# Kernel tuning notes

Hardware: AMD Instinct MI355X
Metric: run time of the kernel (lower is better)

Reference implementation:

```python
import jax, jax.numpy as jnp
import numpy as np
import math

B, S, E = 4, 2048, 1024


def setup_inputs() -> dict:
    key = jax.random.key(0)
    ks = jax.random.split(key, 9)
    x = jax.random.normal(ks[0], (B, S, E), dtype=jnp.float32)
    # causal boolean mask, broadcast over batch: True = keep
    mask = jnp.broadcast_to(jnp.tril(jnp.ones((S, S), dtype=bool)), (B, S, S))
    sc = 1.0 / math.sqrt(E)
    Wq = jax.random.normal(ks[1], (E, E), dtype=jnp.float32) * sc
    bq = jnp.zeros((E,), dtype=jnp.float32)
    Wk = jax.random.normal(ks[2], (E, E), dtype=jnp.float32) * sc
    bk = jnp.zeros((E,), dtype=jnp.float32)
    Wv = jax.random.normal(ks[3], (E, E), dtype=jnp.float32) * sc
    bv = jnp.zeros((E,), dtype=jnp.float32)
    gamma = jnp.ones((E,), dtype=jnp.float32)
    beta = jnp.zeros((E,), dtype=jnp.float32)
    return {"x": x, "mask": mask, "Wq": Wq, "bq": bq, "Wk": Wk, "bk": bk,
            "Wv": Wv, "bv": bv, "gamma": gamma, "beta": beta}


def reference(x, mask, Wq, bq, Wk, bk, Wv, bv, gamma, beta):
    E_ = x.shape[-1]
    q = jnp.einsum('bse,fe->bsf', x, Wq) + bq
    k = jnp.einsum('bse,fe->bsf', x, Wk) + bk
    v = jnp.einsum('bse,fe->bsf', x, Wv) + bv
    scores = jnp.einsum('bqe,bke->bqk', q, k) / jnp.sqrt(jnp.float32(E_))
    scores = jnp.where(mask, scores, -jnp.inf)
    probs = jax.nn.softmax(scores, axis=-1)
    attn = jnp.einsum('bqk,bke->bqe', probs, v)
    y = attn + x
    # LayerNorm over last dim, eps matches torch default 1e-5
    mu = jnp.mean(y, axis=-1, keepdims=True)
    var = jnp.mean(jnp.square(y - mu), axis=-1, keepdims=True)
    return (y - mu) / jnp.sqrt(var + 1e-5) * gamma + beta
```

## Files before the change

kernel.cpp:

```cpp
#include <hip/hip_runtime.h>
#include <hip/hip_bf16.h>
#include <stdint.h>

#define B_ 4
#define S_ 2048
#define E_ 1024
#define BS_ (B_*S_)

using bf16x8 = __attribute__((ext_vector_type(8))) __bf16;
using f32x4  = __attribute__((ext_vector_type(4))) float;

__constant__ int pv_mt[24] = {7,8,9,10,11,12,13,14,15,15,14,6,13,5,12,4,11,3,10,2,9,1,8,0};
__constant__ int pv_ck[24] = {0,0,0,0,0,0,0,0,0, 1, 1,0, 1,0, 1,0, 1,0, 1,0, 1,0, 1,0};

__device__ __forceinline__ unsigned short f2bf(float f) {
  unsigned int u = __float_as_uint(f);
  u += 0x7fffu + ((u >> 16) & 1u);
  return (unsigned short)(u >> 16);
}
__device__ __forceinline__ float bf2f(unsigned short h) {
  return __uint_as_float(((unsigned int)h) << 16);
}

__device__ __forceinline__ void gld16(const unsigned short* g, unsigned short* l) {
  __builtin_amdgcn_global_load_lds((__attribute__((address_space(1))) void*)(void*)g,
                                   (__attribute__((address_space(3))) void*)l, 16, 0, 0);
}

__global__ __launch_bounds__(256) void prep_all(
    const float* __restrict__ x,
    const float* __restrict__ Wq, const float* __restrict__ Wk, const float* __restrict__ Wv,
    const float* __restrict__ bq, const float* __restrict__ bk, const float* __restrict__ bv,
    unsigned short* __restrict__ xb, unsigned short* __restrict__ Wb, float* __restrict__ bb) {
  const int i = blockIdx.x * 256 + threadIdx.x;
  const int nx4 = BS_ * E_ / 4, nw4 = E_ * E_ / 4;
  if (i < nx4) {
    const float4 v = ((const float4*)x)[i];
    ushort4 o;
    o.x = f2bf(v.x); o.y = f2bf(v.y); o.z = f2bf(v.z); o.w = f2bf(v.w);
    ((ushort4*)xb)[i] = o;
  } else if (i < nx4 + 3 * nw4) {
    const int j = i - nx4;
    const int m = j / nw4, jj = j - m * nw4;
    const float* src = (m == 0) ? Wq : (m == 1) ? Wk : Wv;
    const float4 v = ((const float4*)src)[jj];
    ushort4 o;
    o.x = f2bf(v.x); o.y = f2bf(v.y); o.z = f2bf(v.z); o.w = f2bf(v.w);
    ((ushort4*)Wb)[j] = o;
  } else {
    const int j = i - nx4 - 3 * nw4;
    if (j < 3 * E_) bb[j] = (j < E_) ? bq[j] : (j < 2 * E_) ? bk[j - E_] : bv[j - 2 * E_];
  }
}

template<int EPI>
__global__ __launch_bounds__(256, 3) void gemm_bt(
    const unsigned short* __restrict__ A, const unsigned short* __restrict__ Bm,
    float* __restrict__ Cf, float* __restrict__ Cf2,
    unsigned short* __restrict__ Cb, unsigned short* __restrict__ VtOut,
    const float* __restrict__ bias,
    int K, int lda, int ldb, int ldc,
    long sA, long sB, long sC, float scale)
{
  constexpr int BM = 128, BN = 128, BK = 64;
  __shared__ __align__(16) unsigned short As[BM * BK];
  __shared__ __align__(16) unsigned short Bs[BN * BK];

  int mt, nt, ck = 0, bz;
  if (EPI == 1) {
    const int sig = (blockIdx.x & 7) * 68 + (blockIdx.x >> 3);
    bz = sig / 136;
    const int rem = sig - bz * 136;
    const int M = (rem >= 78) ? 3 : (rem >= 36) ? 2 : (rem >= 10) ? 1 : 0;
    const int cumM = (M == 3) ? 78 : (M == 2) ? 36 : (M == 1) ? 10 : 0;
    const int inner = rem - cumM;
    if (inner < 16 * M) {
      const int N = inner >> 4, t2 = inner & 15;
      mt = 4 * M + (t2 >> 2); nt = 4 * N + (t2 & 3);
    } else {
      const int t2 = inner - 16 * M;
      const int ml = (t2 >= 6) ? 3 : (t2 >= 3) ? 2 : (t2 >= 1) ? 1 : 0;
      const int nl = t2 - (ml * (ml + 1)) / 2;
      mt = 4 * M + ml; nt = 4 * M + nl;
    }
  } else if (EPI == 2) {
    mt = pv_mt[blockIdx.y]; ck = pv_ck[blockIdx.y]; nt = blockIdx.x; bz = blockIdx.z;
  } else {
    mt = blockIdx.y; nt = blockIdx.x; bz = blockIdx.z;
  }
  A  += sA * bz;
  Bm += sB * bz;
  const int m0 = mt * BM, n0 = nt * BN;
  const int k0s  = (EPI == 2 && ck) ? 1024 : 0;
  const int kend = (EPI == 2) ? (ck ? m0 + BM : min(1024, m0 + BM)) : K;

  const int t = threadIdx.x;
  const int lane = t & 63, wave = t >> 6;
  const int wr = wave >> 1, wc = wave & 1;
  const int q = lane >> 4, r = lane & 15;

  const int srow   = lane >> 3;
  const int schunk = (lane & 7) ^ srow;
  const long ga0 = (long)(m0 + wave * 32 + srow) * lda + schunk * 8;
  const long gb0 = (long)(n0 + wave * 32 + srow) * ldb + schunk * 8;

  f32x4 acc[4][4] = {};

  for (int k0 = k0s; k0 < kend; k0 += BK) {
#pragma unroll
    for (int s = 0; s < 4; ++s) {
      gld16(A  + ga0 + (long)s * 8 * lda + k0, &As[(wave * 32 + s * 8) * 64]);
      gld16(Bm + gb0 + (long)s * 8 * ldb + k0, &Bs[(wave * 32 + s * 8) * 64]);
    }
    __syncthreads();
#pragma unroll
    for (int kk = 0; kk < BK; kk += 32) {
      bf16x8 af[4], bfr[4];
      const int cq = (kk >> 3) + q;
#pragma unroll
      for (int i = 0; i < 4; ++i) {
        const int row = wr * 64 + i * 16 + r;
        af[i] = *(const bf16x8*)&As[(row * 8 + (cq ^ (r & 7))) * 8];
      }
#pragma unroll
      for (int j = 0; j < 4; ++j) {
        const int row = wc * 64 + j * 16 + r;
        bfr[j] = *(const bf16x8*)&Bs[(row * 8 + (cq ^ (r & 7))) * 8];
      }
#pragma unroll
      for (int i = 0; i < 4; ++i)
#pragma unroll
        for (int j = 0; j < 4; ++j)
          acc[i][j] = __builtin_amdgcn_mfma_f32_16x16x32_bf16(af[i], bfr[j], acc[i][j], 0, 0, 0);
    }
    __syncthreads();
  }

  if (EPI == 0) {
    if (n0 < 2 * E_) {
#pragma unroll
      for (int i = 0; i < 4; ++i)
#pragma unroll
        for (int j = 0; j < 4; ++j) {
          const int col = n0 + wc * 64 + j * 16 + r;
          const float bia = bias[col];
#pragma unroll
          for (int e = 0; e < 4; ++e) {
            const int rowg = m0 + wr * 64 + i * 16 + q * 4 + e;
            Cb[(long)rowg * ldc + col] = f2bf(acc[i][j][e] + bia);
          }
        }
    } else {
      unsigned short* scr = As + wave * 2048;
      const int bb = m0 >> 11;
      const int sbase = (m0 & (S_ - 1)) + wr * 64;
      const float bia = bias[n0 + wc * 64 +  0 + r];
      (void)bia;
#pragma unroll
      for (int j = 0; j < 4; ++j) {
        const int e_base = n0 - 2 * E_ + wc * 64 + j * 16;
        const float bj = bias[n0 + wc * 64 + j * 16 + r];
#pragma unroll
        for (int i = 0; i < 4; ++i) {
          const int c = 2 * i + (q >> 1);
          const int slot = c ^ (r & 7);
          ushort4 o;
          o.x = f2bf(acc[i][j][0] + bj);
          o.y = f2bf(acc[i][j][1] + bj);
          o.z = f2bf(acc[i][j][2] + bj);
          o.w = f2bf(acc[i][j][3] + bj);
          *(ushort4*)&scr[r * 72 + slot * 8 + (q & 1) * 4] = o;
        }
#pragma unroll
        for (int it = 0; it < 2; ++it) {
          const int er = it * 8 + (lane >> 3);
          const int w = lane & 7;
          const bf16x8 vv = *(const bf16x8*)&scr[er * 72 + w * 8];
          const int so = (w ^ (er & 7)) * 8;
          *(bf16x8*)&VtOut[((long)bb * E_ + e_base + er) * S_ + sbase + so] = vv;
        }
      }
    }
  } else if (EPI == 1) {
    Cb += sC * bz;
#pragma unroll
    for (int i = 0; i < 4; ++i)
#pragma unroll
      for (int j = 0; j < 4; ++j) {
        const int col = n0 + wc * 64 + j * 16 + r;
#pragma unroll
        for (int e = 0; e < 4; ++e) {
          const int rowg = m0 + wr * 64 + i * 16 + q * 4 + e;
          Cb[(long)rowg * ldc + col] = f2bf(acc[i][j][e] * scale);
        }
      }
  } else {
    float* dst = (ck ? Cf2 : Cf) + sC * bz;
#pragma unroll
    for (int i = 0; i < 4; ++i)
#pragma unroll
      for (int j = 0; j < 4; ++j) {
        const int col = n0 + wc * 64 + j * 16 + r;
#pragma unroll
        for (int e = 0; e < 4; ++e) {
          const int rowg = m0 + wr * 64 + i * 16 + q * 4 + e;
          dst[(long)rowg * ldc + col] = acc[i][j][e];
        }
      }
  }
}

__global__ __launch_bounds__(256) void softmax_causal(unsigned short* __restrict__ Sc) {
  const int row = blockIdx.x * 4 + (threadIdx.x >> 6);
  const int lane = threadIdx.x & 63;
  const int b = row >> 11, ii = row & (S_ - 1);
  unsigned short* prow = Sc + (long)b * S_ * S_ + (long)ii * S_;
  const int len = ii + 1;
  const int wend = ((ii >> 7) + 1) << 7;
  float v[32];
#pragma unroll
  for (int c = 0; c < 4; ++c) {
    const int base = (c * 64 + lane) * 8;
    if (base < len) {
      const uint4 u = *(const uint4*)&prow[base];
      const unsigned int w[4] = {u.x, u.y, u.z, u.w};
#pragma unroll
      for (int e = 0; e < 8; ++e) {
        const unsigned short h = (unsigned short)(w[e >> 1] >> ((e & 1) * 16));
        v[c * 8 + e] = (base + e < len) ? bf2f(h) : -3.0e38f;
      }
    } else {
#pragma unroll
      for (int e = 0; e < 8; ++e) v[c * 8 + e] = -3.0e38f;
    }
  }
  float mx = -3.0e38f;
#pragma unroll
  for (int i = 0; i < 32; ++i) mx = fmaxf(mx, v[i]);
#pragma unroll
  for (int o = 32; o; o >>= 1) mx = fmaxf(mx, __shfl_xor(mx, o));
  float sum = 0.f;
#pragma unroll
  for (int i = 0; i < 32; ++i) { v[i] = __expf(v[i] - mx); sum += v[i]; }
#pragma unroll
  for (int o = 32; o; o >>= 1) sum += __shfl_xor(sum, o);
  const float inv = 1.0f / sum;
#pragma unroll
  for (int c = 0; c < 4; ++c) {
    const int base = (c * 64 + lane) * 8;
    if (base >= wend) continue;
    uint4 u;
    unsigned int w[4];
#pragma unroll
    for (int p = 0; p < 4; ++p) {
      const unsigned short lo = f2bf(v[c * 8 + p * 2] * inv);
      const unsigned short hi = f2bf(v[c * 8 + p * 2 + 1] * inv);
      w[p] = (unsigned int)lo | ((unsigned int)hi << 16);
    }
    u.x = w[0]; u.y = w[1]; u.z = w[2]; u.w = w[3];
    *(uint4*)&prow[base] = u;
  }
}

__global__ __launch_bounds__(256) void residual_ln(
    const float* __restrict__ attn, const float* __restrict__ attn2,
    const float* __restrict__ x,
    const float* __restrict__ gamma, const float* __restrict__ beta,
    float* __restrict__ out) {
  __shared__ float rs[4], rs2[4];
  const long row = blockIdx.x;
  const int t = threadIdx.x;
  const int lane = t & 63, wave = t >> 6;
  const float4 a  = ((const float4*)(attn + row * E_))[t];
  const float4 xv = ((const float4*)(x + row * E_))[t];
  float4 a2 = make_float4(0.f, 0.f, 0.f, 0.f);
  if ((row & (S_ - 1)) >= 1024) a2 = ((const float4*)(attn2 + row * E_))[t];
  const float y0 = a.x + a2.x + xv.x, y1 = a.y + a2.y + xv.y;
  const float y2 = a.z + a2.z + xv.z, y3 = a.w + a2.w + xv.w;
  float s  = y0 + y1 + y2 + y3;
  float s2 = y0 * y0 + y1 * y1 + y2 * y2 + y3 * y3;
#pragma unroll
  for (int o = 32; o; o >>= 1) { s += __shfl_xor(s, o); s2 += __shfl_xor(s2, o); }
  if (lane == 0) { rs[wave] = s; rs2[wave] = s2; }
  __syncthreads();
  s  = rs[0] + rs[1] + rs[2] + rs[3];
  s2 = rs2[0] + rs2[1] + rs2[2] + rs2[3];
  const float mu  = s * (1.0f / E_);
  const float var = s2 * (1.0f / E_) - mu * mu;
  const float inv = rsqrtf(var + 1e-5f);
  const float4 g  = ((const float4*)gamma)[t];
  const float4 be = ((const float4*)beta)[t];
  float4 o;
  o.x = (y0 - mu) * inv * g.x + be.x;
  o.y = (y1 - mu) * inv * g.y + be.y;
  o.z = (y2 - mu) * inv * g.z + be.z;
  o.w = (y3 - mu) * inv * g.w + be.w;
  ((float4*)(out + row * E_))[t] = o;
}

extern "C" void kernel_launch(void* const* d_in, const int* in_sizes, int n_in,
                              void* d_out, int out_size, void* d_ws, size_t ws_size,
                              hipStream_t stream) {
  const float* x  = (const float*)d_in[0];
  const float* Wq = (const float*)d_in[2];
  const float* bq = (const float*)d_in[3];
  const float* Wk = (const float*)d_in[4];
  const float* bk = (const float*)d_in[5];
  const float* Wv = (const float*)d_in[6];
  const float* bv = (const float*)d_in[7];
  const float* gamma = (const float*)d_in[8];
  const float* beta  = (const float*)d_in[9];
  float* out = (float*)d_out;

  char* ws = (char*)d_ws;
  size_t off = 0;
  auto alloc = [&](size_t bytes) { char* p = ws + off; off += (bytes + 255) & ~(size_t)255; return p; };
  unsigned short* xb    = (unsigned short*)alloc((size_t)BS_ * E_ * 2);
  unsigned short* Wqkvb = (unsigned short*)alloc((size_t)3 * E_ * E_ * 2);
  float*          bqkv  = (float*)alloc((size_t)3 * E_ * 4);
  unsigned short* Cqkv  = (unsigned short*)alloc((size_t)BS_ * 2 * E_ * 2);
  unsigned short* Vt    = (unsigned short*)alloc((size_t)BS_ * E_ * 2);
  unsigned short* Sc    = (unsigned short*)alloc((size_t)B_ * S_ * S_ * 2);
  float*          attn2 = (float*)alloc((size_t)BS_ * E_ * 4);
  float* attn = (float*)Cqkv;

  const int nprep = BS_ * E_ / 4 + 3 * E_ * E_ / 4 + 3 * E_;
  prep_all<<<dim3((nprep + 255) / 256), 256, 0, stream>>>(x, Wq, Wk, Wv, bq, bk, bv, xb, Wqkvb, bqkv);

  dim3 g1(3 * E_ / 128, BS_ / 128, 1);
  gemm_bt<0><<<g1, 256, 0, stream>>>(xb, Wqkvb, nullptr, nullptr, Cqkv, Vt, bqkv,
                                     E_, E_, E_, 2 * E_, 0, 0, 0, 1.f);

  gemm_bt<1><<<dim3(544), 256, 0, stream>>>(Cqkv, Cqkv + E_, nullptr, nullptr, Sc, nullptr, nullptr,
                                            E_, 2 * E_, 2 * E_, S_,
                                            (long)S_ * 2 * E_, (long)S_ * 2 * E_, (long)S_ * S_,
                                            0.03125f);

  softmax_causal<<<dim3(BS_ / 4), 256, 0, stream>>>(Sc);

  dim3 g3(E_ / 128, 24, B_);
  gemm_bt<2><<<g3, 256, 0, stream>>>(Sc, Vt, attn, attn2, nullptr, nullptr, nullptr,
                                     S_, S_, S_, E_,
                                     (long)S_ * S_, (long)S_ * E_, (long)S_ * E_, 1.f);

  residual_ln<<<dim3(BS_), 256, 0, stream>>>(attn, attn2, x, gamma, beta, out);
}
```

Baseline: 277.1 us.

## Fuse causal softmax into QK and PV GEMM epilogues, drop softmax kernel

The score GEMM epilogue now applies the causal mask and writes unnormalized exp(score), without subtracting a row max; the exponent is clamped at 60. Per-row sums are accumulated with atomics into a row-sum buffer that the prep kernel zeroes. The PV GEMM divides by that sum in its epilogue and writes bf16 partial outputs, which the LayerNorm kernel then reads. This removes the separate softmax pass over the score matrix and halves the bytes of the attention intermediates. In exchange it adds atomics and loses numerical safety for large logits, since it relies on scores staying small.

```diff
diff --git a/kernel.cpp b/kernel.cpp
--- a/kernel.cpp
+++ b/kernel.cpp
@@ -31,7 +31,8 @@
     const float* __restrict__ x,
     const float* __restrict__ Wq, const float* __restrict__ Wk, const float* __restrict__ Wv,
     const float* __restrict__ bq, const float* __restrict__ bk, const float* __restrict__ bv,
-    unsigned short* __restrict__ xb, unsigned short* __restrict__ Wb, float* __restrict__ bb) {
+    unsigned short* __restrict__ xb, unsigned short* __restrict__ Wb, float* __restrict__ bb,
+    float* __restrict__ lz) {
   const int i = blockIdx.x * 256 + threadIdx.x;
   const int nx4 = BS_ * E_ / 4, nw4 = E_ * E_ / 4;
   if (i < nx4) {
@@ -50,13 +51,14 @@
   } else {
     const int j = i - nx4 - 3 * nw4;
     if (j < 3 * E_) bb[j] = (j < E_) ? bq[j] : (j < 2 * E_) ? bk[j - E_] : bv[j - 2 * E_];
+    else { const int k = j - 3 * E_; if (k < BS_) lz[k] = 0.f; }
   }
 }
 
 template<int EPI>
 __global__ __launch_bounds__(256, 3) void gemm_bt(
     const unsigned short* __restrict__ A, const unsigned short* __restrict__ Bm,
-    float* __restrict__ Cf, float* __restrict__ Cf2,
+    float* __restrict__ Cf,
     unsigned short* __restrict__ Cb, unsigned short* __restrict__ VtOut,
     const float* __restrict__ bias,
     int K, int lda, int ldb, int ldc,
@@ -154,8 +156,6 @@
       unsigned short* scr = As + wave * 2048;
       const int bb = m0 >> 11;
       const int sbase = (m0 & (S_ - 1)) + wr * 64;
-      const float bia = bias[n0 + wc * 64 +  0 + r];
-      (void)bia;
 #pragma unroll
       for (int j = 0; j < 4; ++j) {
         const int e_base = n0 - 2 * E_ + wc * 64 + j * 16;
@@ -183,87 +183,52 @@
     }
   } else if (EPI == 1) {
     Cb += sC * bz;
-#pragma unroll
-    for (int i = 0; i < 4; ++i)
+    float* lv = Cf + (long)bz * S_;
+#pragma unroll
+    for (int i = 0; i < 4; ++i) {
+      float rs[4] = {0.f, 0.f, 0.f, 0.f};
 #pragma unroll
       for (int j = 0; j < 4; ++j) {
         const int col = n0 + wc * 64 + j * 16 + r;
 #pragma unroll
         for (int e = 0; e < 4; ++e) {
           const int rowg = m0 + wr * 64 + i * 16 + q * 4 + e;
-          Cb[(long)rowg * ldc + col] = f2bf(acc[i][j][e] * scale);
+          float p = 0.f;
+          if (col <= rowg) p = __expf(fminf(acc[i][j][e] * scale, 60.f));
+          Cb[(long)rowg * ldc + col] = f2bf(p);
+          rs[e] += p;
         }
       }
+#pragma unroll
+      for (int e = 0; e < 4; ++e) {
+        float s = rs[e];
+        s += __shfl_xor(s, 1); s += __shfl_xor(s, 2);
+        s += __shfl_xor(s, 4); s += __shfl_xor(s, 8);
+        if (r == 0) atomicAdd(&lv[m0 + wr * 64 + i * 16 + q * 4 + e], s);
+      }
+    }
   } else {
-    float* dst = (ck ? Cf2 : Cf) + sC * bz;
-#pragma unroll
-    for (int i = 0; i < 4; ++i)
+    const float* lv = Cf + (long)bz * S_;
+    unsigned short* dst = (ck ? VtOut : Cb) + sC * bz;
+#pragma unroll
+    for (int i = 0; i < 4; ++i) {
+      const int rb = m0 + wr * 64 + i * 16 + q * 4;
+      const float4 l4 = *(const float4*)&lv[rb];
+      const float r0 = 1.f / l4.x, r1 = 1.f / l4.y, r2 = 1.f / l4.z, r3 = 1.f / l4.w;
 #pragma unroll
       for (int j = 0; j < 4; ++j) {
         const int col = n0 + wc * 64 + j * 16 + r;
-#pragma unroll
-        for (int e = 0; e < 4; ++e) {
-          const int rowg = m0 + wr * 64 + i * 16 + q * 4 + e;
-          dst[(long)rowg * ldc + col] = acc[i][j][e];
-        }
-      }
+        dst[(long)(rb + 0) * ldc + col] = f2bf(acc[i][j][0] * r0);
+        dst[(long)(rb + 1) * ldc + col] = f2bf(acc[i][j][1] * r1);
+        dst[(long)(rb + 2) * ldc + col] = f2bf(acc[i][j][2] * r2);
+        dst[(long)(rb + 3) * ldc + col] = f2bf(acc[i][j][3] * r3);
+      }
+    }
   }
 }
 
-__global__ __launch_bounds__(256) void softmax_causal(unsigned short* __restrict__ Sc) {
-  const int row = blockIdx.x * 4 + (threadIdx.x >> 6);
-  const int lane = threadIdx.x & 63;
-  const int b = row >> 11, ii = row & (S_ - 1);
-  unsigned short* prow = Sc + (long)b * S_ * S_ + (long)ii * S_;
-  const int len = ii + 1;
-  const int wend = ((ii >> 7) + 1) << 7;
-  float v[32];
-#pragma unroll
-  for (int c = 0; c < 4; ++c) {
-    const int base = (c * 64 + lane) * 8;
-    if (base < len) {
-      const uint4 u = *(const uint4*)&prow[base];
-      const unsigned int w[4] = {u.x, u.y, u.z, u.w};
-#pragma unroll
-      for (int e = 0; e < 8; ++e) {
-        const unsigned short h = (unsigned short)(w[e >> 1] >> ((e & 1) * 16));
-        v[c * 8 + e] = (base + e < len) ? bf2f(h) : -3.0e38f;
-      }
-    } else {
-#pragma unroll
-      for (int e = 0; e < 8; ++e) v[c * 8 + e] = -3.0e38f;
-    }
-  }
-  float mx = -3.0e38f;
-#pragma unroll
-  for (int i = 0; i < 32; ++i) mx = fmaxf(mx, v[i]);
-#pragma unroll
-  for (int o = 32; o; o >>= 1) mx = fmaxf(mx, __shfl_xor(mx, o));
-  float sum = 0.f;
-#pragma unroll
-  for (int i = 0; i < 32; ++i) { v[i] = __expf(v[i] - mx); sum += v[i]; }
-#pragma unroll
-  for (int o = 32; o; o >>= 1) sum += __shfl_xor(sum, o);
-  const float inv = 1.0f / sum;
-#pragma unroll
-  for (int c = 0; c < 4; ++c) {
-    const int base = (c * 64 + lane) * 8;
-    if (base >= wend) continue;
-    uint4 u;
-    unsigned int w[4];
-#pragma unroll
-    for (int p = 0; p < 4; ++p) {
-      const unsigned short lo = f2bf(v[c * 8 + p * 2] * inv);
-      const unsigned short hi = f2bf(v[c * 8 + p * 2 + 1] * inv);
-      w[p] = (unsigned int)lo | ((unsigned int)hi << 16);
-    }
-    u.x = w[0]; u.y = w[1]; u.z = w[2]; u.w = w[3];
-    *(uint4*)&prow[base] = u;
-  }
-}
-
 __global__ __launch_bounds__(256) void residual_ln(
-    const float* __restrict__ attn, const float* __restrict__ attn2,
+    const unsigned short* __restrict__ attn, const unsigned short* __restrict__ attn2,
     const float* __restrict__ x,
     const float* __restrict__ gamma, const float* __restrict__ beta,
     float* __restrict__ out) {
@@ -271,12 +236,14 @@
   const long row = blockIdx.x;
   const int t = threadIdx.x;
   const int lane = t & 63, wave = t >> 6;
-  const float4 a  = ((const float4*)(attn + row * E_))[t];
+  const ushort4 a  = ((const ushort4*)(attn + row * E_))[t];
   const float4 xv = ((const float4*)(x + row * E_))[t];
-  float4 a2 = make_float4(0.f, 0.f, 0.f, 0.f);
-  if ((row & (S_ - 1)) >= 1024) a2 = ((const float4*)(attn2 + row * E_))[t];
-  const float y0 = a.x + a2.x + xv.x, y1 = a.y + a2.y + xv.y;
-  const float y2 = a.z + a2.z + xv.z, y3 = a.w + a2.w + xv.w;
+  ushort4 b2 = make_ushort4(0, 0, 0, 0);
+  if ((row & (S_ - 1)) >= 1024) b2 = ((const ushort4*)(attn2 + row * E_))[t];
+  const float y0 = bf2f(a.x) + bf2f(b2.x) + xv.x;
+  const float y1 = bf2f(a.y) + bf2f(b2.y) + xv.y;
+  const float y2 = bf2f(a.z) + bf2f(b2.z) + xv.z;
+  const float y3 = bf2f(a.w) + bf2f(b2.w) + xv.w;
   float s  = y0 + y1 + y2 + y3;
   float s2 = y0 * y0 + y1 * y1 + y2 * y2 + y3 * y3;
 #pragma unroll
@@ -321,25 +288,25 @@
   unsigned short* Cqkv  = (unsigned short*)alloc((size_t)BS_ * 2 * E_ * 2);
   unsigned short* Vt    = (unsigned short*)alloc((size_t)BS_ * E_ * 2);
   unsigned short* Sc    = (unsigned short*)alloc((size_t)B_ * S_ * S_ * 2);
-  float*          attn2 = (float*)alloc((size_t)BS_ * E_ * 4);
-  float* attn = (float*)Cqkv;
-
-  const int nprep = BS_ * E_ / 4 + 3 * E_ * E_ / 4 + 3 * E_;
-  prep_all<<<dim3((nprep + 255) / 256), 256, 0, stream>>>(x, Wq, Wk, Wv, bq, bk, bv, xb, Wqkvb, bqkv);
+  float*          lrow  = (float*)alloc((size_t)BS_ * 4);
+  unsigned short* attn  = (unsigned short*)Cqkv;
+  unsigned short* attn2 = (unsigned short*)Cqkv + (size_t)BS_ * E_;
+
+  const int nprep = BS_ * E_ / 4 + 3 * E_ * E_ / 4 + 3 * E_ + BS_;
+  prep_all<<<dim3((nprep + 255) / 256), 256, 0, stream>>>(x, Wq, Wk, Wv, bq, bk, bv,
+                                                          xb, Wqkvb, bqkv, lrow);
 
   dim3 g1(3 * E_ / 128, BS_ / 128, 1);
-  gemm_bt<0><<<g1, 256, 0, stream>>>(xb, Wqkvb, nullptr, nullptr, Cqkv, Vt, bqkv,
+  gemm_bt<0><<<g1, 256, 0, stream>>>(xb, Wqkvb, nullptr, Cqkv, Vt, bqkv,
                                      E_, E_, E_, 2 * E_, 0, 0, 0, 1.f);
 
-  gemm_bt<1><<<dim3(544), 256, 0, stream>>>(Cqkv, Cqkv + E_, nullptr, nullptr, Sc, nullptr, nullptr,
+  gemm_bt<1><<<dim3(544), 256, 0, stream>>>(Cqkv, Cqkv + E_, lrow, Sc, nullptr, nullptr,
                                             E_, 2 * E_, 2 * E_, S_,
                                             (long)S_ * 2 * E_, (long)S_ * 2 * E_, (long)S_ * S_,
                                             0.03125f);
 
-  softmax_causal<<<dim3(BS_ / 4), 256, 0, stream>>>(Sc);
-
   dim3 g3(E_ / 128, 24, B_);
-  gemm_bt<2><<<g3, 256, 0, stream>>>(Sc, Vt, attn, attn2, nullptr, nullptr, nullptr,
+  gemm_bt<2><<<g3, 256, 0, stream>>>(Sc, Vt, lrow, attn, attn2, nullptr,
                                      S_, S_, S_, E_,
                                      (long)S_ * S_, (long)S_ * E_, (long)S_ * E_, 1.f);
 
```

After: 273.5 us. No clear change (-1.3%).
